# Performance work log

Measured on AMD Instinct MI355X. Metric: run time of the kernel, lower is better.

Reference implementation:

```python
import jax, jax.numpy as jnp
import numpy as np

HIDDEN = 128
SINKHORN_ITERS = 60
TEMPERATURE = 3.0
GAMMA = 0.01
ALPHA = 10.0
NEG_BIG = 1e9


def setup_inputs() -> dict:
    key = jax.random.key(0)
    ks = jax.random.split(key, 12)
    B, N = 16, 512
    points = jax.random.uniform(ks[0], (B, N, 2), dtype=jnp.float32)
    distances = jax.random.uniform(ks[1], (B, N, N), dtype=jnp.float32)
    noise_u = jax.random.uniform(ks[2], (B, N, N), dtype=jnp.float32, minval=1e-6, maxval=1.0 - 1e-6)
    s_emb = 1.0 / np.sqrt(2.0)
    s_h = 1.0 / np.sqrt(HIDDEN)
    W_emb = jax.random.uniform(ks[3], (2, HIDDEN), jnp.float32, -s_emb, s_emb)
    b_emb = jax.random.uniform(ks[4], (HIDDEN,), jnp.float32, -s_emb, s_emb)
    W1 = jax.random.uniform(ks[5], (HIDDEN, HIDDEN), jnp.float32, -s_h, s_h)
    b1 = jax.random.uniform(ks[6], (HIDDEN,), jnp.float32, -s_h, s_h)
    W2 = jax.random.uniform(ks[7], (HIDDEN, HIDDEN), jnp.float32, -s_h, s_h)
    b2 = jax.random.uniform(ks[8], (HIDDEN,), jnp.float32, -s_h, s_h)
    W3 = jax.random.uniform(ks[9], (HIDDEN, HIDDEN), jnp.float32, -s_h, s_h)
    b3 = jax.random.uniform(ks[10], (HIDDEN,), jnp.float32, -s_h, s_h)
    return {"points": points, "distances": distances, "noise_u": noise_u,
            "W_emb": W_emb, "b_emb": b_emb, "W1": W1, "b1": b1,
            "W2": W2, "b2": b2, "W3": W3, "b3": b3}


def _gcn(x, adjacency, W, b):
    # bmm(adjacency, x) then linear + relu
    neighbor = jnp.einsum('bnm,bmd->bnd', adjacency, x)
    return jax.nn.relu(neighbor @ W + b)


def _sinkhorn(P):
    def body(P, _):
        P = P / jnp.sum(P, axis=1, keepdims=True)  # column normalize
        P = P / jnp.sum(P, axis=2, keepdims=True)  # row normalize
        return P, None
    P, _ = jax.lax.scan(body, P, None, length=SINKHORN_ITERS)
    return P


def reference(points, distances, noise_u, W_emb, b_emb, W1, b1, W2, b2, W3, b3):
    B, N, _ = points.shape
    adjacency = jnp.exp(-distances)                      # (B,N,N)
    x = points @ W_emb + b_emb                           # (B,N,H)
    x = _gcn(x, adjacency, W1, b1)
    x = _gcn(x, adjacency, W2, b2)
    x = _gcn(x, adjacency, W3, b3)
    logits = jnp.einsum('bnd,bmd->bnm', x, x)            # (B,N,N)
    logits = logits - NEG_BIG * jnp.eye(N, dtype=logits.dtype)[None]
    logits = ALPHA * jnp.tanh(logits)
    epsilon = -jnp.log(-jnp.log(noise_u))                # Gumbel noise
    y = (logits + GAMMA * epsilon) / TEMPERATURE
    P = jax.nn.softmax(y, axis=-1)
    return _sinkhorn(P)
```

## Files before the change

### kernel.cpp

```cpp
#include <hip/hip_runtime.h>

#define BB 16
#define NN 512
#define HH 128
#define SB 32
#define RB 16

#define SCOPE_AGENT __HIP_MEMORY_SCOPE_AGENT

typedef _Float16 f16x8 __attribute__((ext_vector_type(8)));
typedef _Float16 f16x4 __attribute__((ext_vector_type(4)));
typedef float    f32x4 __attribute__((ext_vector_type(4)));

template <bool EMB>
__global__ __launch_bounds__(256) void gcn_kernel(
    const float* __restrict__ dist, const _Float16* __restrict__ xTin,
    const float* __restrict__ pts, const float* __restrict__ Wemb,
    const float* __restrict__ bemb,
    const float* __restrict__ W, const float* __restrict__ bias,
    _Float16* __restrict__ xfout, _Float16* __restrict__ xTout,
    unsigned int* __restrict__ ctrlz)
{
  __shared__ _Float16 Al[32][40];
  __shared__ _Float16 Bl[128][40];
  __shared__ _Float16 Cl[32][136];
  __shared__ _Float16 Wl[128][136];

  const int bid = blockIdx.x;
  const int mt = bid & 15, b = bid >> 4;
  const int tid = threadIdx.x;
  const int row0 = mt * 32;

  if (EMB) {
    int idx = bid * 256 + tid;
    if (idx < 49152) ctrlz[idx] = 0u;
  }

  #pragma unroll
  for (int rep = 0; rep < 64; ++rep) {
    const int idx = rep * 256 + tid;
    const int k = idx >> 7, n = idx & 127;
    Wl[n][k] = (_Float16)W[(size_t)k * HH + n];
  }

  const float* Ab = dist + ((size_t)b * NN + row0) * NN;
  const _Float16* xTb = EMB ? nullptr : (xTin + (size_t)b * HH * NN);

  const int wv = tid >> 6, lane = tid & 63;
  const int wm = wv >> 1, wn = wv & 1;
  const int fr = lane & 15, fo = lane >> 4;

  float we0a = 0.f, we1a = 0.f, ba = 0.f, we0b = 0.f, we1b = 0.f, bb2 = 0.f;
  const int n0 = tid >> 2, q4 = tid & 3;
  if (EMB) {
    we0a = Wemb[n0];      we1a = Wemb[HH + n0];      ba  = bemb[n0];
    we0b = Wemb[n0 + 64]; we1b = Wemb[HH + n0 + 64]; bb2 = bemb[n0 + 64];
  }

  f32x4 acc[4] = {};

  for (int k0 = 0; k0 < NN; k0 += 32) {
    {
      const int r = tid >> 3, q = tid & 7;
      float4 v = *reinterpret_cast<const float4*>(&Ab[(size_t)r * NN + k0 + q * 4]);
      f16x4 h;
      h[0] = (_Float16)__expf(-v.x); h[1] = (_Float16)__expf(-v.y);
      h[2] = (_Float16)__expf(-v.z); h[3] = (_Float16)__expf(-v.w);
      *reinterpret_cast<f16x4*>(&Al[r][q * 4]) = h;
    }
    if (!EMB) {
      #pragma unroll
      for (int it = 0; it < 2; ++it) {
        const int slot = it * 256 + tid;
        const int n = slot >> 2, q = slot & 3;
        f16x8 v = *reinterpret_cast<const f16x8*>(&xTb[(size_t)n * NN + k0 + q * 8]);
        *reinterpret_cast<f16x8*>(&Bl[n][q * 8]) = v;
      }
    } else {
      float2 pv[8];
      #pragma unroll
      for (int e = 0; e < 8; ++e)
        pv[e] = *reinterpret_cast<const float2*>(
            &pts[((size_t)b * NN + k0 + q4 * 8 + e) * 2]);
      f16x8 va, vb;
      #pragma unroll
      for (int e = 0; e < 8; ++e) {
        va[e] = (_Float16)fmaf(pv[e].x, we0a, fmaf(pv[e].y, we1a, ba));
        vb[e] = (_Float16)fmaf(pv[e].x, we0b, fmaf(pv[e].y, we1b, bb2));
      }
      *reinterpret_cast<f16x8*>(&Bl[n0][q4 * 8]) = va;
      *reinterpret_cast<f16x8*>(&Bl[n0 + 64][q4 * 8]) = vb;
    }
    __syncthreads();
    f16x8 af = *reinterpret_cast<const f16x8*>(&Al[wm * 16 + fr][fo * 8]);
    #pragma unroll
    for (int nt = 0; nt < 4; ++nt) {
      f16x8 bf = *reinterpret_cast<const f16x8*>(&Bl[wn * 64 + nt * 16 + fr][fo * 8]);
      acc[nt] = __builtin_amdgcn_mfma_f32_16x16x32_f16(af, bf, acc[nt], 0, 0, 0);
    }
    __syncthreads();
  }

  #pragma unroll
  for (int nt = 0; nt < 4; ++nt) {
    const int col = wn * 64 + nt * 16 + fr;
    #pragma unroll
    for (int m = 0; m < 4; ++m)
      Cl[wm * 16 + fo * 4 + m][col] = (_Float16)(acc[nt][m] * 0x1p-10f);
  }
  __syncthreads();

  f32x4 acc2[4] = {};
  #pragma unroll
  for (int ks = 0; ks < 4; ++ks) {
    f16x8 af2 = *reinterpret_cast<const f16x8*>(&Cl[wm * 16 + fr][ks * 32 + fo * 8]);
    #pragma unroll
    for (int nt = 0; nt < 4; ++nt) {
      f16x8 bf2 = *reinterpret_cast<const f16x8*>(&Wl[wn * 64 + nt * 16 + fr][ks * 32 + fo * 8]);
      acc2[nt] = __builtin_amdgcn_mfma_f32_16x16x32_f16(af2, bf2, acc2[nt], 0, 0, 0);
    }
  }

  _Float16* xfb = xfout + (size_t)b * NN * HH;
  _Float16* xTb2 = xTout + (size_t)b * HH * NN;
  #pragma unroll
  for (int nt = 0; nt < 4; ++nt) {
    const int col = wn * 64 + nt * 16 + fr;
    const float bv = bias[col];
    const int rowb = row0 + wm * 16 + fo * 4;
    f16x4 hc;
    #pragma unroll
    for (int m = 0; m < 4; ++m) {
      float v = fmaxf(fmaf(acc2[nt][m], 1024.0f, bv), 0.0f);
      hc[m] = (_Float16)v;
      xfb[(size_t)(rowb + m) * HH + col] = (_Float16)v;
    }
    *reinterpret_cast<f16x4*>(&xTb2[(size_t)col * NN + rowb]) = hc;
  }
}

__global__ __launch_bounds__(256) void sinkhorn_kernel(
    const _Float16* __restrict__ xf, const float* __restrict__ noise,
    float* __restrict__ cacc, unsigned int* __restrict__ flags,
    float* __restrict__ out)
{
  __shared__ float Pl[RB][513];
  __shared__ float cl[512];
  __shared__ float rl[RB];
  __shared__ float red[16][17];
  __shared__ float wmax[4];
  __shared__ int stopf;

  const int bid = blockIdx.x;
  const int b = bid >> 5, s = bid & 31;
  const int tid = threadIdx.x;
  const int i0 = s * RB;

  const _Float16* xb = xf + (size_t)b * NN * HH;
  const float* nzb = noise + ((size_t)b * NN + i0) * NN;
  const int wv = tid >> 6, lane = tid & 63;
  const int fr = lane & 15, fo = lane >> 4;
  const int jbase = wv * 128;

  {
    float rowpart[4] = {0.f, 0.f, 0.f, 0.f};
    for (int jt = 0; jt < 8; ++jt) {
      const int jcol = jbase + jt * 16 + fr;
      f32x4 acc = {};
      #pragma unroll
      for (int ks = 0; ks < 4; ++ks) {
        f16x8 af = *reinterpret_cast<const f16x8*>(
            &xb[(size_t)(i0 + fr) * HH + ks * 32 + fo * 8]);
        f16x8 bf = *reinterpret_cast<const f16x8*>(
            &xb[(size_t)jcol * HH + ks * 32 + fo * 8]);
        acc = __builtin_amdgcn_mfma_f32_16x16x32_f16(af, bf, acc, 0, 0, 0);
      }
      #pragma unroll
      for (int m = 0; m < 4; ++m) {
        const int r = fo * 4 + m;
        float sv = acc[m];
        if (i0 + r == jcol) sv -= 1e9f;
        float th = 1.0f - 2.0f / (__expf(2.0f * sv) + 1.0f);
        float u  = nzb[(size_t)r * NN + jcol];
        float eps = -__logf(-__logf(u));
        float e = __expf((10.0f * th + 0.01f * eps) * (1.0f / 3.0f));
        Pl[r][jcol] = e;
        rowpart[m] += e;
      }
    }
    #pragma unroll
    for (int m = 0; m < 4; ++m) {
      float v = rowpart[m];
      v += __shfl_xor(v, 1); v += __shfl_xor(v, 2);
      v += __shfl_xor(v, 4); v += __shfl_xor(v, 8);
      if (fr == 0) red[wv][fo * 4 + m] = v;
    }
  }
  cl[tid] = 1.0f; cl[tid + 256] = 1.0f;
  __syncthreads();
  if (tid < RB)
    rl[tid] = 1.0f / (red[0][tid] + red[1][tid] + red[2][tid] + red[3][tid]);
  __syncthreads();

  auto row_update = [&]() {
    const int i = tid & 15, ch = tid >> 4;
    const int j0 = ch * 32, st = (ch * 8) & 31;
    float p = 0.0f;
    #pragma unroll
    for (int q = 0; q < 32; ++q) {
      const int j = j0 + ((q + st) & 31);
      p = fmaf(Pl[i][j], cl[j], p);
    }
    red[ch][i] = p;
    __syncthreads();
    if (tid < RB) {
      float v = 0.0f;
      #pragma unroll
      for (int q = 0; q < 16; ++q) v += red[q][tid];
      rl[tid] = 1.0f / v;
    }
    __syncthreads();
  };

  unsigned int* myflag = flags + (size_t)(b * SB + s) * 64;
  float* ca0 = cacc + (size_t)b * 512;
  float* ca1 = cacc + (size_t)(BB + b) * 512;
  float pA0 = 0.f, pA1 = 0.f, pB0 = 0.f, pB1 = 0.f;
  unsigned int convbit = 0;

  for (int it = 0; it < 60; ++it) {
    float* ca  = (it & 1) ? ca1 : ca0;
    float& pv0 = (it & 1) ? pB0 : pA0;
    float& pv1 = (it & 1) ? pB1 : pA1;

    float u0 = 0.0f, u1 = 0.0f;
    #pragma unroll
    for (int i2 = 0; i2 < RB; ++i2) {
      const float rv = rl[i2];
      u0 = fmaf(Pl[i2][tid],       rv, u0);
      u1 = fmaf(Pl[i2][tid + 256], rv, u1);
    }
    __hip_atomic_fetch_add(&ca[tid],       u0 - pv0, __ATOMIC_RELAXED, SCOPE_AGENT);
    __hip_atomic_fetch_add(&ca[tid + 256], u1 - pv1, __ATOMIC_RELAXED, SCOPE_AGENT);
    pv0 = u0; pv1 = u1;
    __syncthreads();

    if (tid == 0)
      __hip_atomic_store(myflag, ((unsigned int)(it + 1) << 1) | convbit,
                         __ATOMIC_RELAXED, SCOPE_AGENT);
    if (tid < 64) {
      unsigned int v = 3u;
      if (tid < SB) {
        const unsigned int* fp = flags + (size_t)(b * SB + tid) * 64;
        do {
          v = __hip_atomic_load(fp, __ATOMIC_RELAXED, SCOPE_AGENT);
          if ((v >> 1) >= (unsigned int)(it + 1)) break;
          __builtin_amdgcn_s_sleep(1);
        } while (true);
      }
      unsigned long long m = __ballot((v & 1u) != 0u);
      if (tid == 0) stopf = ((m & 0xFFFFFFFFull) == 0xFFFFFFFFull) ? 1 : 0;
    }
    __syncthreads();
    if (stopf) break;

    float t0 = __hip_atomic_load(&ca[tid],       __ATOMIC_RELAXED, SCOPE_AGENT);
    float t1 = __hip_atomic_load(&ca[tid + 256], __ATOMIC_RELAXED, SCOPE_AGENT);
    float d = fmaxf(fabsf(fmaf(t0, cl[tid], -1.0f)),
                    fabsf(fmaf(t1, cl[tid + 256], -1.0f)));
    #pragma unroll
    for (int off = 32; off >= 1; off >>= 1) d = fmaxf(d, __shfl_xor(d, off));
    if ((tid & 63) == 0) wmax[tid >> 6] = d;
    cl[tid] = 1.0f / t0; cl[tid + 256] = 1.0f / t1;
    __syncthreads();
    const float dm = fmaxf(fmaxf(wmax[0], wmax[1]), fmaxf(wmax[2], wmax[3]));
    convbit = (dm < 1e-3f) ? 1u : 0u;
    row_update();
  }

  float* Ob = out + ((size_t)b * NN + i0) * NN;
  #pragma unroll
  for (int i = 0; i < RB; ++i) {
    const float rv = rl[i];
    Ob[(size_t)i * NN + tid]       = rv * Pl[i][tid]       * cl[tid];
    Ob[(size_t)i * NN + tid + 256] = rv * Pl[i][tid + 256] * cl[tid + 256];
  }
}

extern "C" void kernel_launch(void* const* d_in, const int* in_sizes, int n_in,
                              void* d_out, int out_size, void* d_ws, size_t ws_size,
                              hipStream_t stream)
{
  const float* points = (const float*)d_in[0];
  const float* dist   = (const float*)d_in[1];
  const float* noise  = (const float*)d_in[2];
  const float* Wemb   = (const float*)d_in[3];
  const float* bemb   = (const float*)d_in[4];
  const float* W1 = (const float*)d_in[5]; const float* b1 = (const float*)d_in[6];
  const float* W2 = (const float*)d_in[7]; const float* b2 = (const float*)d_in[8];
  const float* W3 = (const float*)d_in[9]; const float* b3 = (const float*)d_in[10];
  float* out = (float*)d_out;

  char* ws = (char*)d_ws;
  _Float16* xfA = (_Float16*)ws;
  _Float16* xTA = (_Float16*)(ws + (2u << 20));
  _Float16* xfB = (_Float16*)(ws + (4u << 20));
  _Float16* xTB = (_Float16*)(ws + (6u << 20));
  char* ctrl = ws + (8u << 20);
  float*        cacc  = (float*)ctrl;
  unsigned int* flags = (unsigned int*)(ctrl + (64u << 10));

  gcn_kernel<true><<<256, 256, 0, stream>>>(dist, nullptr, points, Wemb, bemb,
                                            W1, b1, xfA, xTA, (unsigned int*)ctrl);
  gcn_kernel<false><<<256, 256, 0, stream>>>(dist, xTA, nullptr, nullptr, nullptr,
                                             W2, b2, xfB, xTB, nullptr);
  gcn_kernel<false><<<256, 256, 0, stream>>>(dist, xTB, nullptr, nullptr, nullptr,
                                             W3, b3, xfA, xTA, nullptr);

  const _Float16* xfc = xfA; const float* nzc = noise;
  float* caccP = cacc; unsigned int* flagsP = flags; float* outP = out;
  void* args[] = {(void*)&xfc, (void*)&nzc, (void*)&caccP, (void*)&flagsP, (void*)&outP};
  hipLaunchCooperativeKernel(reinterpret_cast<void*>(sinkhorn_kernel),
                             dim3(BB * SB), dim3(256), args, 0, stream);
}
```

Before: 96.19 us.

## Cache fp16 adjacency in workspace, double-buffer GCN tiles, hoist A fragments, vectorize output

Result: faster. 85.62 us (-11.0%).

```diff
diff --git a/kernel.cpp b/kernel.cpp
--- a/kernel.cpp
+++ b/kernel.cpp
@@ -14,15 +14,16 @@
 
 template <bool EMB>
 __global__ __launch_bounds__(256) void gcn_kernel(
-    const float* __restrict__ dist, const _Float16* __restrict__ xTin,
+    const float* __restrict__ dist, _Float16* __restrict__ adjws,
+    const _Float16* __restrict__ xTin,
     const float* __restrict__ pts, const float* __restrict__ Wemb,
     const float* __restrict__ bemb,
     const float* __restrict__ W, const float* __restrict__ bias,
     _Float16* __restrict__ xfout, _Float16* __restrict__ xTout,
     unsigned int* __restrict__ ctrlz)
 {
-  __shared__ _Float16 Al[32][40];
-  __shared__ _Float16 Bl[128][40];
+  __shared__ _Float16 Al2[2][32][40];
+  __shared__ _Float16 Bl2[2][128][40];
   __shared__ _Float16 Cl[32][136];
   __shared__ _Float16 Wl[128][136];
 
@@ -44,6 +45,8 @@
   }
 
   const float* Ab = dist + ((size_t)b * NN + row0) * NN;
+  _Float16* adjwb = adjws + ((size_t)b * NN + row0) * NN;
+  const _Float16* adjrb = adjws + ((size_t)b * NN + row0) * NN;
   const _Float16* xTb = EMB ? nullptr : (xTin + (size_t)b * HH * NN);
 
   const int wv = tid >> 6, lane = tid & 63;
@@ -57,24 +60,29 @@
     we0b = Wemb[n0 + 64]; we1b = Wemb[HH + n0 + 64]; bb2 = bemb[n0 + 64];
   }
 
-  f32x4 acc[4] = {};
-
-  for (int k0 = 0; k0 < NN; k0 += 32) {
-    {
+  auto stageA = [&](int buf, int k0) {
+    if (EMB) {
       const int r = tid >> 3, q = tid & 7;
       float4 v = *reinterpret_cast<const float4*>(&Ab[(size_t)r * NN + k0 + q * 4]);
       f16x4 h;
       h[0] = (_Float16)__expf(-v.x); h[1] = (_Float16)__expf(-v.y);
       h[2] = (_Float16)__expf(-v.z); h[3] = (_Float16)__expf(-v.w);
-      *reinterpret_cast<f16x4*>(&Al[r][q * 4]) = h;
-    }
+      *reinterpret_cast<f16x4*>(&Al2[buf][r][q * 4]) = h;
+      *reinterpret_cast<f16x4*>(&adjwb[(size_t)r * NN + k0 + q * 4]) = h;
+    } else {
+      const int r = tid >> 3, q = tid & 7;
+      *reinterpret_cast<f16x4*>(&Al2[buf][r][q * 4]) =
+          *reinterpret_cast<const f16x4*>(&adjrb[(size_t)r * NN + k0 + q * 4]);
+    }
+  };
+  auto stageB = [&](int buf, int k0) {
     if (!EMB) {
       #pragma unroll
       for (int it = 0; it < 2; ++it) {
         const int slot = it * 256 + tid;
         const int n = slot >> 2, q = slot & 3;
         f16x8 v = *reinterpret_cast<const f16x8*>(&xTb[(size_t)n * NN + k0 + q * 8]);
-        *reinterpret_cast<f16x8*>(&Bl[n][q * 8]) = v;
+        *reinterpret_cast<f16x8*>(&Bl2[buf][n][q * 8]) = v;
       }
     } else {
       float2 pv[8];
@@ -88,14 +96,27 @@
         va[e] = (_Float16)fmaf(pv[e].x, we0a, fmaf(pv[e].y, we1a, ba));
         vb[e] = (_Float16)fmaf(pv[e].x, we0b, fmaf(pv[e].y, we1b, bb2));
       }
-      *reinterpret_cast<f16x8*>(&Bl[n0][q4 * 8]) = va;
-      *reinterpret_cast<f16x8*>(&Bl[n0 + 64][q4 * 8]) = vb;
-    }
-    __syncthreads();
-    f16x8 af = *reinterpret_cast<const f16x8*>(&Al[wm * 16 + fr][fo * 8]);
+      *reinterpret_cast<f16x8*>(&Bl2[buf][n0][q4 * 8]) = va;
+      *reinterpret_cast<f16x8*>(&Bl2[buf][n0 + 64][q4 * 8]) = vb;
+    }
+  };
+
+  f32x4 acc[4] = {};
+
+  stageA(0, 0);
+  stageB(0, 0);
+  __syncthreads();
+
+  for (int k0 = 0; k0 < NN; k0 += 32) {
+    const int cur = (k0 >> 5) & 1;
+    if (k0 + 32 < NN) {
+      stageA(cur ^ 1, k0 + 32);
+      stageB(cur ^ 1, k0 + 32);
+    }
+    f16x8 af = *reinterpret_cast<const f16x8*>(&Al2[cur][wm * 16 + fr][fo * 8]);
     #pragma unroll
     for (int nt = 0; nt < 4; ++nt) {
-      f16x8 bf = *reinterpret_cast<const f16x8*>(&Bl[wn * 64 + nt * 16 + fr][fo * 8]);
+      f16x8 bf = *reinterpret_cast<const f16x8*>(&Bl2[cur][wn * 64 + nt * 16 + fr][fo * 8]);
       acc[nt] = __builtin_amdgcn_mfma_f32_16x16x32_f16(af, bf, acc[nt], 0, 0, 0);
     }
     __syncthreads();
@@ -163,17 +184,21 @@
   const int jbase = wv * 128;
 
   {
+    f16x8 af[4];
+    #pragma unroll
+    for (int ks = 0; ks < 4; ++ks)
+      af[ks] = *reinterpret_cast<const f16x8*>(
+          &xb[(size_t)(i0 + fr) * HH + ks * 32 + fo * 8]);
+
     float rowpart[4] = {0.f, 0.f, 0.f, 0.f};
     for (int jt = 0; jt < 8; ++jt) {
       const int jcol = jbase + jt * 16 + fr;
       f32x4 acc = {};
       #pragma unroll
       for (int ks = 0; ks < 4; ++ks) {
-        f16x8 af = *reinterpret_cast<const f16x8*>(
-            &xb[(size_t)(i0 + fr) * HH + ks * 32 + fo * 8]);
         f16x8 bf = *reinterpret_cast<const f16x8*>(
             &xb[(size_t)jcol * HH + ks * 32 + fo * 8]);
-        acc = __builtin_amdgcn_mfma_f32_16x16x32_f16(af, bf, acc, 0, 0, 0);
+        acc = __builtin_amdgcn_mfma_f32_16x16x32_f16(af[ks], bf, acc, 0, 0, 0);
       }
       #pragma unroll
       for (int m = 0; m < 4; ++m) {
@@ -280,10 +305,16 @@
 
   float* Ob = out + ((size_t)b * NN + i0) * NN;
   #pragma unroll
-  for (int i = 0; i < RB; ++i) {
-    const float rv = rl[i];
-    Ob[(size_t)i * NN + tid]       = rv * Pl[i][tid]       * cl[tid];
-    Ob[(size_t)i * NN + tid + 256] = rv * Pl[i][tid + 256] * cl[tid + 256];
+  for (int rep = 0; rep < 8; ++rep) {
+    const int row = rep * 2 + (tid >> 7);
+    const int c4  = (tid & 127) * 4;
+    const float rv = rl[row];
+    float4 o;
+    o.x = rv * Pl[row][c4 + 0] * cl[c4 + 0];
+    o.y = rv * Pl[row][c4 + 1] * cl[c4 + 1];
+    o.z = rv * Pl[row][c4 + 2] * cl[c4 + 2];
+    o.w = rv * Pl[row][c4 + 3] * cl[c4 + 3];
+    *reinterpret_cast<float4*>(&Ob[(size_t)row * NN + c4]) = o;
   }
 }
 
@@ -306,15 +337,16 @@
   _Float16* xTA = (_Float16*)(ws + (2u << 20));
   _Float16* xfB = (_Float16*)(ws + (4u << 20));
   _Float16* xTB = (_Float16*)(ws + (6u << 20));
-  char* ctrl = ws + (8u << 20);
+  _Float16* adjw = (_Float16*)(ws + (8u << 20));
+  char* ctrl = ws + (16u << 20);
   float*        cacc  = (float*)ctrl;
   unsigned int* flags = (unsigned int*)(ctrl + (64u << 10));
 
-  gcn_kernel<true><<<256, 256, 0, stream>>>(dist, nullptr, points, Wemb, bemb,
+  gcn_kernel<true><<<256, 256, 0, stream>>>(dist, adjw, nullptr, points, Wemb, bemb,
                                             W1, b1, xfA, xTA, (unsigned int*)ctrl);
-  gcn_kernel<false><<<256, 256, 0, stream>>>(dist, xTA, nullptr, nullptr, nullptr,
+  gcn_kernel<false><<<256, 256, 0, stream>>>(nullptr, adjw, xTA, nullptr, nullptr, nullptr,
                                              W2, b2, xfB, xTB, nullptr);
-  gcn_kernel<false><<<256, 256, 0, stream>>>(dist, xTB, nullptr, nullptr, nullptr,
+  gcn_kernel<false><<<256, 256, 0, stream>>>(nullptr, adjw, xTB, nullptr, nullptr, nullptr,
                                              W3, b3, xfA, xTA, nullptr);
 
   const _Float16* xfc = xfA; const float* nzc = noise;
```
